# Kernel optimization log

Measured on AMD Instinct MI355X. Metric: run time of the kernel, lower is better.

## Reference

```python
import jax, jax.numpy as jnp
import numpy as np

N, D, R, T, E = 4096, 1024, 92, 32, 8192
SCALE = float(np.sqrt(2.0 / 7.0))  # matches torch.rand(...) * sqrt(2/7)


def setup_inputs() -> dict:
    key = jax.random.key(0)
    ks = jax.random.split(key, 7)
    x = jax.random.normal(ks[0], (N, D), dtype=jnp.float32)
    edge_tok = jax.random.randint(ks[1], (E,), 0, N)
    edge_rel = jax.random.randint(ks[2], (E,), 0, R)
    W_stack = jax.random.uniform(ks[3], (R, D, D), dtype=jnp.float32) * SCALE  # depWeights
    B_stack = jnp.ones((R, D), dtype=jnp.float32)                              # depBias
    W_self = jax.random.uniform(ks[4], (D, D), dtype=jnp.float32) * SCALE      # self.weight
    b_self = jnp.ones((D,), dtype=jnp.float32)                                 # self.bias
    W_tag = jax.random.normal(ks[5], (D, T), dtype=jnp.float32) * 0.02         # hidden2tag
    b_tag = jnp.zeros((T,), dtype=jnp.float32)
    return {"x": x, "W_self": W_self, "b_self": b_self, "W_stack": W_stack,
            "B_stack": B_stack, "W_tag": W_tag, "b_tag": b_tag,
            "edge_tok": edge_tok, "edge_rel": edge_rel}


def reference(x, W_self, b_self, W_stack, B_stack, W_tag, b_tag, edge_tok, edge_rel):
    n, r = x.shape[0], W_stack.shape[0]
    # C[i, r] = number of dependency edges of token i with relation r
    C = jnp.zeros((n, r), dtype=x.dtype).at[edge_tok, edge_rel].add(jnp.asarray(1.0, x.dtype))
    self_out = x @ W_self + b_self  # [N, D]
    # accum_i = self_out_i + sum_{dep in deps(i)} (x_i @ W_dep + b_dep)
    #         = self_out_i + sum_r C[i, r] * (x_i @ W_r) + (C @ B_stack)_i
    def body(acc, wc):
        Wr, Cr = wc  # Wr: [D, D], Cr: [N]
        return acc + Cr[:, None] * (x @ Wr), None
    dep_out, _ = jax.lax.scan(body, jnp.zeros_like(self_out), (W_stack, C.T))
    h = jax.nn.relu(self_out + dep_out + C @ B_stack)  # [N, D]
    tag_scores = jax.nn.log_softmax(h @ W_tag + b_tag, axis=1)  # [N, T]
    return tag_scores, h
```

## Files before the change

### kernel.cpp

```cpp
#include <hip/hip_runtime.h>
#include <hip/hip_bf16.h>
#include <math.h>

#define N_TOK 4096
#define D_DIM 1024
#define R_REL 92
#define T_TAG 32
#define E_EDGE 8192
#define SELF_R 127
#define GRID_ITEMS 192

typedef short bf16x8 __attribute__((ext_vector_type(8)));
typedef float f32x4 __attribute__((ext_vector_type(4)));

union Pk8 { uint4 q; unsigned short s[8]; };
union Pk4 { uint2 d; unsigned short s[4]; };

__device__ __forceinline__ unsigned short f2bf(float f) {
    union { __hip_bfloat16 b; unsigned short u; } c;
    c.b = __float2bfloat16(f);
    return c.u;
}


__global__ __launch_bounds__(1024) void k_setup(const int* __restrict__ rel,
                                                int* __restrict__ ws) {
    __shared__ int cnt[128], offL[128], cur[128], sh[128];
    int t = threadIdx.x;
    if (t < 128) cnt[t] = 0;
    __syncthreads();
    #pragma unroll
    for (int i = 0; i < E_EDGE / 1024; ++i)
        atomicAdd(&cnt[rel[i * 1024 + t]], 1);
    __syncthreads();
    int c = (t < 128) ? cnt[t] : 0;
    int v = c;
    if (t < 128) sh[t] = v;
    __syncthreads();
    for (int st = 1; st < 128; st <<= 1) {
        int add = (t >= st && t < 128) ? sh[t - st] : 0;
        __syncthreads();
        if (t < 128) { v += add; sh[t] = v; }
        __syncthreads();
    }
    if (t < 128) { offL[t] = v - c; ws[256 + t] = v - c; ws[t] = c; cur[t] = 0; }
    int ch = (t < R_REL) ? ((c + 127) >> 7) : 0;
    int v2 = ch;
    if (t < 128) sh[t] = v2;
    __syncthreads();
    for (int st = 1; st < 128; st <<= 1) {
        int add = (t >= st && t < 128) ? sh[t - st] : 0;
        __syncthreads();
        if (t < 128) { v2 += add; sh[t] = v2; }
        __syncthreads();
    }
    if (t < 32) ws[512 + t] = (SELF_R << 16) | t;
    if (t < R_REL) {
        int excl = v2 - ch;
        for (int j = 0; j < ch; ++j)
            ws[512 + 32 + excl + j] = (t << 16) | j;
    }
    if (t == 127) ws[384] = 32 + v2;
    __syncthreads();
    #pragma unroll
    for (int i = 0; i < E_EDGE / 1024; ++i) {
        int e = i * 1024 + t;
        int r = rel[e];
        int pos = offL[r] + atomicAdd(&cur[r], 1);
        ws[1024 + pos] = e;
    }
}

__global__ __launch_bounds__(256, 2) void k_fused(const float* __restrict__ x,
                                                  const float* __restrict__ Wself,
                                                  const float* __restrict__ bself,
                                                  const float* __restrict__ Wst,
                                                  const float* __restrict__ Bst,
                                                  const int* __restrict__ etok,
                                                  const int* __restrict__ ws,
                                                  float* __restrict__ out_h) {
    if ((int)blockIdx.x >= ws[384]) return;
    int item = ws[512 + blockIdx.x];
    int r = item >> 16, chunk = item & 0xFFFF;
    int m0 = chunk * 128;
    int valid;
    const float* Wbase;
    const float* bias;
    bool is_self = (r == SELF_R);
    int off0 = 0;
    if (is_self) {
        valid = 128;
        Wbase = Wself;
        bias = bself;
    } else {
        int cnt = ws[r];
        off0 = ws[256 + r];
        valid = cnt - m0; if (valid > 128) valid = 128;
        Wbase = Wst + (size_t)r * D_DIM * D_DIM;
        bias = Bst + (size_t)r * D_DIM;
    }

    __shared__ unsigned short Al[128 * 64];
    __shared__ unsigned short Bl[128 * 64];
    __shared__ int toks[128];
    char* Alb = (char*)Al;
    char* Blb = (char*)Bl;
    int t = threadIdx.x;
    if (t < 128) {
        int tok;
        if (is_self) tok = m0 + t;
        else tok = (t < valid) ? etok[ws[1024 + off0 + m0 + t]] : 0;
        toks[t] = tok;
    }
    __syncthreads();

    int gn0 = blockIdx.y * 128;
    int w = t >> 6, l = t & 63;
    int lr = l & 15, lg = l >> 4;
    int wm = (w >> 1) * 64, wn = (w & 1) * 64;
    int ar = t >> 4, ac = t & 15;
    int tok_s[8];
    #pragma unroll
    for (int s = 0; s < 8; ++s) tok_s[s] = toks[s * 16 + ar];
    int bn = (w & 1) * 64 + l;
    int bkb = (w >> 1) * 32;
    const float* wcol = Wbase + gn0 + bn;

    float4 pa[8];
    float pb[32];

    #pragma unroll
    for (int s = 0; s < 8; ++s)
        pa[s] = *(const float4*)(x + (size_t)tok_s[s] * D_DIM + ac * 4);
    #pragma unroll
    for (int s = 0; s < 4; ++s)
        #pragma unroll
        for (int i = 0; i < 8; ++i)
            pb[s * 8 + i] = wcol[(size_t)(bkb + s * 8 + i) * D_DIM];
    #pragma unroll
    for (int s = 0; s < 8; ++s) {
        int row = s * 16 + ar;
        Pk4 u;
        u.s[0] = f2bf(pa[s].x); u.s[1] = f2bf(pa[s].y);
        u.s[2] = f2bf(pa[s].z); u.s[3] = f2bf(pa[s].w);
        *(uint2*)(Alb + row * 128 + ((ac * 8) ^ ((row & 7) << 4))) = u.d;
    }
    #pragma unroll
    for (int s = 0; s < 4; ++s) {
        Pk8 u;
        #pragma unroll
        for (int i = 0; i < 8; ++i) u.s[i] = f2bf(pb[s * 8 + i]);
        *(uint4*)(Blb + bn * 128 + ((bkb * 2 + s * 16) ^ ((bn & 7) << 4))) = u.q;
    }
    __syncthreads();

    f32x4 acc[4][4] = {};
    for (int k0 = 0; k0 < D_DIM; k0 += 64) {
        bool pf = (k0 + 64 < D_DIM);
        if (pf) {
            int kn = k0 + 64;
            #pragma unroll
            for (int s = 0; s < 8; ++s)
                pa[s] = *(const float4*)(x + (size_t)tok_s[s] * D_DIM + kn + ac * 4);
            #pragma unroll
            for (int s = 0; s < 4; ++s)
                #pragma unroll
                for (int i = 0; i < 8; ++i)
                    pb[s * 8 + i] = wcol[(size_t)(kn + bkb + s * 8 + i) * D_DIM];
        }
        #pragma unroll
        for (int kk = 0; kk < 2; ++kk) {
            int koff = kk * 64 + lg * 16;
            bf16x8 af[4], bfr[4];
            #pragma unroll
            for (int mi = 0; mi < 4; ++mi)
                af[mi] = *(const bf16x8*)(Alb + (wm + mi * 16 + lr) * 128 +
                                          (koff ^ ((lr & 7) << 4)));
            #pragma unroll
            for (int ni = 0; ni < 4; ++ni)
                bfr[ni] = *(const bf16x8*)(Blb + (wn + ni * 16 + lr) * 128 +
                                           (koff ^ ((lr & 7) << 4)));
            #pragma unroll
            for (int mi = 0; mi < 4; ++mi)
                #pragma unroll
                for (int ni = 0; ni < 4; ++ni)
                    acc[mi][ni] = __builtin_amdgcn_mfma_f32_16x16x32_bf16(
                        af[mi], bfr[ni], acc[mi][ni], 0, 0, 0);
        }
        __syncthreads();
        if (pf) {
            #pragma unroll
            for (int s = 0; s < 8; ++s) {
                int row = s * 16 + ar;
                Pk4 u;
                u.s[0] = f2bf(pa[s].x); u.s[1] = f2bf(pa[s].y);
                u.s[2] = f2bf(pa[s].z); u.s[3] = f2bf(pa[s].w);
                *(uint2*)(Alb + row * 128 + ((ac * 8) ^ ((row & 7) << 4))) = u.d;
            }
            #pragma unroll
            for (int s = 0; s < 4; ++s) {
                Pk8 u;
                #pragma unroll
                for (int i = 0; i < 8; ++i) u.s[i] = f2bf(pb[s * 8 + i]);
                *(uint4*)(Blb + bn * 128 + ((bkb * 2 + s * 16) ^ ((bn & 7) << 4))) = u.q;
            }
            __syncthreads();
        }
    }
    float bb[4];
    #pragma unroll
    for (int ni = 0; ni < 4; ++ni) bb[ni] = bias[gn0 + wn + ni * 16 + lr];
    #pragma unroll
    for (int mi = 0; mi < 4; ++mi)
        #pragma unroll
        for (int j = 0; j < 4; ++j) {
            int rl = wm + mi * 16 + lg * 4 + j;
            if (rl < valid) {
                float* dst = out_h + (size_t)toks[rl] * D_DIM + gn0 + wn + lr;
                #pragma unroll
                for (int ni = 0; ni < 4; ++ni)
                    atomicAdd(dst + ni * 16, acc[mi][ni][j] + bb[ni]);
            }
        }
}

__global__ __launch_bounds__(256) void k_tag(float* __restrict__ out_h,
                                             const float* __restrict__ Wt,
                                             const float* __restrict__ bt,
                                             float* __restrict__ out_tag) {
    __shared__ unsigned short Al[64 * 64];
    __shared__ unsigned short Bl[32 * 64];
    char* Alb = (char*)Al;
    char* Blb = (char*)Bl;
    int tok0 = blockIdx.x * 64;
    int t = threadIdx.x;
    int w = t >> 6, l = t & 63, lr = l & 15, lg = l >> 4;
    int wm = w * 16;
    int ar = t >> 4, ac = t & 15;
    int bn = t & 31, kh = t >> 5;
    f32x4 acc[2] = {};
    for (int k0 = 0; k0 < D_DIM; k0 += 64) {
        __syncthreads();
        #pragma unroll
        for (int s = 0; s < 4; ++s) {
            int row = s * 16 + ar;
            float* hp = out_h + (size_t)(tok0 + row) * D_DIM + k0 + ac * 4;
            float4 v = *(float4*)hp;
            v.x = fmaxf(v.x, 0.f); v.y = fmaxf(v.y, 0.f);
            v.z = fmaxf(v.z, 0.f); v.w = fmaxf(v.w, 0.f);
            *(float4*)hp = v;
            Pk4 u;
            u.s[0] = f2bf(v.x); u.s[1] = f2bf(v.y);
            u.s[2] = f2bf(v.z); u.s[3] = f2bf(v.w);
            *(uint2*)(Alb + row * 128 + ((ac * 8) ^ ((row & 7) << 4))) = u.d;
        }
        {
            Pk8 u;
            #pragma unroll
            for (int i = 0; i < 8; ++i)
                u.s[i] = f2bf(Wt[(size_t)(k0 + kh * 8 + i) * T_TAG + bn]);
            *(uint4*)(Blb + bn * 128 + ((kh * 16) ^ ((bn & 7) << 4))) = u.q;
        }
        __syncthreads();
        #pragma unroll
        for (int kk = 0; kk < 2; ++kk) {
            int koff = kk * 64 + lg * 16;
            bf16x8 af = *(const bf16x8*)(Alb + (wm + lr) * 128 +
                                         (koff ^ ((lr & 7) << 4)));
            #pragma unroll
            for (int ni = 0; ni < 2; ++ni) {
                bf16x8 bfr = *(const bf16x8*)(Blb + (ni * 16 + lr) * 128 +
                                              (koff ^ ((lr & 7) << 4)));
                acc[ni] = __builtin_amdgcn_mfma_f32_16x16x32_bf16(
                    af, bfr, acc[ni], 0, 0, 0);
            }
        }
    }
    float bt0 = bt[lr], bt1 = bt[16 + lr];
    #pragma unroll
    for (int j = 0; j < 4; ++j) {
        float v0 = acc[0][j] + bt0;
        float v1 = acc[1][j] + bt1;
        float m = fmaxf(v0, v1);
        #pragma unroll
        for (int s = 1; s < 16; s <<= 1) m = fmaxf(m, __shfl_xor(m, s));
        float sum = expf(v0 - m) + expf(v1 - m);
        #pragma unroll
        for (int s = 1; s < 16; s <<= 1) sum += __shfl_xor(sum, s);
        float lse = m + logf(sum);
        int row = tok0 + wm + lg * 4 + j;
        out_tag[(size_t)row * T_TAG + lr] = v0 - lse;
        out_tag[(size_t)row * T_TAG + 16 + lr] = v1 - lse;
    }
}

extern "C" void kernel_launch(void* const* d_in, const int* in_sizes, int n_in,
                              void* d_out, int out_size, void* d_ws, size_t ws_size,
                              hipStream_t stream) {
    const float* x     = (const float*)d_in[0];
    const float* Wself = (const float*)d_in[1];
    const float* bself = (const float*)d_in[2];
    const float* Wst   = (const float*)d_in[3];
    const float* Bst   = (const float*)d_in[4];
    const float* Wtag  = (const float*)d_in[5];
    const float* btag  = (const float*)d_in[6];
    const int*   etok  = (const int*)d_in[7];
    const int*   erel  = (const int*)d_in[8];
    float* out_tag = (float*)d_out;
    float* out_h   = (float*)d_out + (size_t)N_TOK * T_TAG;
    int* ws = (int*)d_ws;

    hipMemsetAsync(out_h, 0, (size_t)N_TOK * D_DIM * sizeof(float), stream);
    k_setup<<<1, 1024, 0, stream>>>(erel, ws);
    k_fused<<<dim3(GRID_ITEMS, D_DIM / 128), 256, 0, stream>>>(
        x, Wself, bself, Wst, Bst, etok, ws, out_h);
    k_tag<<<N_TOK / 64, 256, 0, stream>>>(out_h, Wtag, btag, out_tag);
}
```

Measured before the change: 165.5 us.

## Replace atomic scatter-add with per-edge scratch rows and deterministic per-token reduce

The fused GEMM kernel now writes each edge's output row (and the self rows) to a scratch buffer with plain stores instead of doing float atomicAdds into h. The setup kernel additionally builds a CSR of edges grouped by token, and a new reduce kernel sums each token's self row plus its edge rows, applies ReLU, and writes h. This removes the memset of h and the atomic contention, and moves ReLU out of the tag kernel. In exchange it adds about 12K rows x 4KB of scratch writes and reads, plus an extra kernel launch.

```diff
diff --git a/kernel.cpp b/kernel.cpp
--- a/kernel.cpp
+++ b/kernel.cpp
@@ -10,6 +10,7 @@
 #define SELF_R 127
 #define GRID_ITEMS 192
 
+
 typedef short bf16x8 __attribute__((ext_vector_type(8)));
 typedef float f32x4 __attribute__((ext_vector_type(4)));
 
@@ -22,16 +23,25 @@
     return c.u;
 }
 
-
 __global__ __launch_bounds__(1024) void k_setup(const int* __restrict__ rel,
+                                                const int* __restrict__ tokv,
                                                 int* __restrict__ ws) {
-    __shared__ int cnt[128], offL[128], cur[128], sh[128];
+    __shared__ int cnt[128], offL[128], cur[128];
+    __shared__ int sh[1024];
+    __shared__ int tcnt[4096], toff[4096];
     int t = threadIdx.x;
-    if (t < 128) cnt[t] = 0;
-    __syncthreads();
-    #pragma unroll
-    for (int i = 0; i < E_EDGE / 1024; ++i)
-        atomicAdd(&cnt[rel[i * 1024 + t]], 1);
+    if (t < 128) { cnt[t] = 0; cur[t] = 0; }
+    #pragma unroll
+    for (int i = 0; i < 4; ++i) tcnt[i * 1024 + t] = 0;
+    __syncthreads();
+    int er[8], et[8];
+    #pragma unroll
+    for (int i = 0; i < 8; ++i) {
+        er[i] = rel[i * 1024 + t];
+        et[i] = tokv[i * 1024 + t];
+        atomicAdd(&cnt[er[i]], 1);
+        atomicAdd(&tcnt[et[i]], 1);
+    }
     __syncthreads();
     int c = (t < 128) ? cnt[t] : 0;
     int v = c;
@@ -43,7 +53,7 @@
         if (t < 128) { v += add; sh[t] = v; }
         __syncthreads();
     }
-    if (t < 128) { offL[t] = v - c; ws[256 + t] = v - c; ws[t] = c; cur[t] = 0; }
+    if (t < 128) { offL[t] = v - c; ws[256 + t] = v - c; ws[t] = c; }
     int ch = (t < R_REL) ? ((c + 127) >> 7) : 0;
     int v2 = ch;
     if (t < 128) sh[t] = v2;
@@ -61,13 +71,38 @@
             ws[512 + 32 + excl + j] = (t << 16) | j;
     }
     if (t == 127) ws[384] = 32 + v2;
-    __syncthreads();
-    #pragma unroll
-    for (int i = 0; i < E_EDGE / 1024; ++i) {
-        int e = i * 1024 + t;
-        int r = rel[e];
-        int pos = offL[r] + atomicAdd(&cur[r], 1);
-        ws[1024 + pos] = e;
+    int s0 = tcnt[4 * t + 0], s1 = tcnt[4 * t + 1];
+    int s2 = tcnt[4 * t + 2], s3 = tcnt[4 * t + 3];
+    int sum4 = s0 + s1 + s2 + s3;
+    int vv = sum4;
+    sh[t] = vv;
+    __syncthreads();
+    for (int st = 1; st < 1024; st <<= 1) {
+        int add = (t >= st) ? sh[t - st] : 0;
+        __syncthreads();
+        vv += add; sh[t] = vv;
+        __syncthreads();
+    }
+    int ex = vv - sum4;
+    toff[4 * t + 0] = ex;
+    toff[4 * t + 1] = ex + s0;
+    toff[4 * t + 2] = ex + s0 + s1;
+    toff[4 * t + 3] = ex + s0 + s1 + s2;
+    ws[17408 + 4 * t + 0] = toff[4 * t + 0];
+    ws[17408 + 4 * t + 1] = toff[4 * t + 1];
+    ws[17408 + 4 * t + 2] = toff[4 * t + 2];
+    ws[17408 + 4 * t + 3] = toff[4 * t + 3];
+    if (t == 1023) ws[17408 + 4096] = vv;
+    __syncthreads();
+    #pragma unroll
+    for (int i = 0; i < 4; ++i) tcnt[i * 1024 + t] = 0;
+    __syncthreads();
+    #pragma unroll
+    for (int i = 0; i < 8; ++i) {
+        int pos = offL[er[i]] + atomicAdd(&cur[er[i]], 1);
+        ws[1024 + pos] = et[i];
+        int q = toff[et[i]] + atomicAdd(&tcnt[et[i]], 1);
+        ws[22528 + q] = pos;
     }
 }
 
@@ -76,9 +111,8 @@
                                                   const float* __restrict__ bself,
                                                   const float* __restrict__ Wst,
                                                   const float* __restrict__ Bst,
-                                                  const int* __restrict__ etok,
                                                   const int* __restrict__ ws,
-                                                  float* __restrict__ out_h) {
+                                                  float* __restrict__ scratch) {
     if ((int)blockIdx.x >= ws[384]) return;
     int item = ws[512 + blockIdx.x];
     int r = item >> 16, chunk = item & 0xFFFF;
@@ -99,6 +133,7 @@
         Wbase = Wst + (size_t)r * D_DIM * D_DIM;
         bias = Bst + (size_t)r * D_DIM;
     }
+    int srow_base = is_self ? (8192 + m0) : (off0 + m0);
 
     __shared__ unsigned short Al[128 * 64];
     __shared__ unsigned short Bl[128 * 64];
@@ -109,7 +144,7 @@
     if (t < 128) {
         int tok;
         if (is_self) tok = m0 + t;
-        else tok = (t < valid) ? etok[ws[1024 + off0 + m0 + t]] : 0;
+        else tok = (t < valid) ? ws[1024 + off0 + m0 + t] : 0;
         toks[t] = tok;
     }
     __syncthreads();
@@ -216,15 +251,32 @@
         for (int j = 0; j < 4; ++j) {
             int rl = wm + mi * 16 + lg * 4 + j;
             if (rl < valid) {
-                float* dst = out_h + (size_t)toks[rl] * D_DIM + gn0 + wn + lr;
+                float* dst = scratch + (size_t)(srow_base + rl) * D_DIM + gn0 + wn + lr;
                 #pragma unroll
                 for (int ni = 0; ni < 4; ++ni)
-                    atomicAdd(dst + ni * 16, acc[mi][ni][j] + bb[ni]);
+                    dst[ni * 16] = acc[mi][ni][j] + bb[ni];
             }
         }
 }
 
-__global__ __launch_bounds__(256) void k_tag(float* __restrict__ out_h,
+__global__ __launch_bounds__(256) void k_reduce(const int* __restrict__ ws,
+                                                const float* __restrict__ scratch,
+                                                float* __restrict__ out_h) {
+    int tok = blockIdx.x;
+    int t = threadIdx.x;
+    int j0 = ws[17408 + tok], j1 = ws[17408 + tok + 1];
+    float4 a = *(const float4*)(scratch + (size_t)(8192 + tok) * D_DIM + t * 4);
+    for (int j = j0; j < j1; ++j) {
+        int p = ws[22528 + j];
+        float4 d = *(const float4*)(scratch + (size_t)p * D_DIM + t * 4);
+        a.x += d.x; a.y += d.y; a.z += d.z; a.w += d.w;
+    }
+    a.x = fmaxf(a.x, 0.f); a.y = fmaxf(a.y, 0.f);
+    a.z = fmaxf(a.z, 0.f); a.w = fmaxf(a.w, 0.f);
+    *(float4*)(out_h + (size_t)tok * D_DIM + t * 4) = a;
+}
+
+__global__ __launch_bounds__(256) void k_tag(const float* __restrict__ out_h,
                                              const float* __restrict__ Wt,
                                              const float* __restrict__ bt,
                                              float* __restrict__ out_tag) {
@@ -244,11 +296,8 @@
         #pragma unroll
         for (int s = 0; s < 4; ++s) {
             int row = s * 16 + ar;
-            float* hp = out_h + (size_t)(tok0 + row) * D_DIM + k0 + ac * 4;
-            float4 v = *(float4*)hp;
-            v.x = fmaxf(v.x, 0.f); v.y = fmaxf(v.y, 0.f);
-            v.z = fmaxf(v.z, 0.f); v.w = fmaxf(v.w, 0.f);
-            *(float4*)hp = v;
+            const float* hp = out_h + (size_t)(tok0 + row) * D_DIM + k0 + ac * 4;
+            float4 v = *(const float4*)hp;
             Pk4 u;
             u.s[0] = f2bf(v.x); u.s[1] = f2bf(v.y);
             u.s[2] = f2bf(v.z); u.s[3] = f2bf(v.w);
@@ -309,10 +358,11 @@
     float* out_tag = (float*)d_out;
     float* out_h   = (float*)d_out + (size_t)N_TOK * T_TAG;
     int* ws = (int*)d_ws;
-
-    hipMemsetAsync(out_h, 0, (size_t)N_TOK * D_DIM * sizeof(float), stream);
-    k_setup<<<1, 1024, 0, stream>>>(erel, ws);
+    float* scratch = (float*)d_ws + 32768;
+
+    k_setup<<<1, 1024, 0, stream>>>(erel, etok, ws);
     k_fused<<<dim3(GRID_ITEMS, D_DIM / 128), 256, 0, stream>>>(
-        x, Wself, bself, Wst, Bst, etok, ws, out_h);
+        x, Wself, bself, Wst, Bst, ws, scratch);
+    k_reduce<<<N_TOK, 256, 0, stream>>>(ws, scratch, out_h);
     k_tag<<<N_TOK / 64, 256, 0, stream>>>(out_h, Wtag, btag, out_tag);
 }
```

Result: faster. 158.2 us (-4.4%).
